# Optimization experiments

Measured on AMD Instinct MI355X. Metric: run time of the kernel, lower is better.

## Reference

```python
import jax, jax.numpy as jnp
import numpy as np

HID = 2048      # hidden_size
NH = 16         # num_attention_heads
QLR = 1536      # q_lora_rank
KVLR = 512      # kv_lora_rank
DN = 128        # qk_nope_head_dim
DR = 64         # qk_rope_head_dim
DQK = DN + DR   # qk_head_dim = 192
DV = 128        # v_head_dim
EPS = 1e-6
THETA = 10000.0
B, T = 2, 2048


def rmsnorm(x, scale):
    return x * jax.lax.rsqrt(jnp.mean(x * x, axis=-1, keepdims=True) + EPS) * scale


def rope(x, positions):
    # x: [B, T, h, d]; NeoX-style rotate-half RoPE on the rope slice only
    d = x.shape[-1]
    inv_freq = 1.0 / (THETA ** (jnp.arange(0, d, 2, dtype=jnp.float32) / d))
    ang = positions.astype(jnp.float32)[..., None] * inv_freq       # [B, T, d/2]
    cos = jnp.cos(ang)[:, :, None, :]
    sin = jnp.sin(ang)[:, :, None, :]
    x1, x2 = jnp.split(x, 2, axis=-1)
    return jnp.concatenate([x1 * cos - x2 * sin, x2 * cos + x1 * sin], axis=-1).astype(x.dtype)


def setup_inputs() -> dict:
    key = jax.random.key(0)
    ks = jax.random.split(key, 8)
    s = 0.02
    x = jax.random.normal(ks[0], (B, T, HID), dtype=jnp.float32)
    attention_mask = jnp.ones((B, T), dtype=bool)
    positions = jnp.broadcast_to(jnp.arange(T, dtype=jnp.int32), (B, T))
    wqa = jax.random.normal(ks[1], (HID, QLR), dtype=jnp.float32) * s
    qa_scale = jnp.ones((QLR,), dtype=jnp.float32)
    wqb = jax.random.normal(ks[2], (QLR, NH * DQK), dtype=jnp.float32) * s
    wkva = jax.random.normal(ks[3], (HID, KVLR + DR), dtype=jnp.float32) * s
    kva_scale = jnp.ones((KVLR,), dtype=jnp.float32)
    wkvb = jax.random.normal(ks[4], (KVLR, NH * (DN + DV)), dtype=jnp.float32) * s
    wo = jax.random.normal(ks[5], (NH * DV, HID), dtype=jnp.float32) * s
    return {"x": x, "attention_mask": attention_mask, "positions": positions,
            "wqa": wqa, "qa_scale": qa_scale, "wqb": wqb,
            "wkva": wkva, "kva_scale": kva_scale, "wkvb": wkvb, "wo": wo}


def reference(x, attention_mask, positions, wqa, qa_scale, wqb, wkva, kva_scale, wkvb, wo):
    Bv, Tv, _ = x.shape
    # low-rank Q: hid -> q_lora_rank -> rmsnorm -> heads*qk_head_dim
    q = (rmsnorm(x @ wqa, qa_scale) @ wqb).reshape(Bv, Tv, NH, DQK)
    q_pass, q_rot = q[..., :DN], q[..., DN:]
    # compressed KV + shared rope key
    ckv = x @ wkva                                    # [B, T, KVLR + DR]
    kv_lat, k_rot = ckv[..., :KVLR], ckv[..., KVLR:].reshape(Bv, Tv, 1, DR)
    kv = (rmsnorm(kv_lat, kva_scale) @ wkvb).reshape(Bv, Tv, NH, DN + DV)
    k_pass, v = kv[..., :DN], kv[..., DN:]
    # decoupled RoPE on rope slice only
    q_rot = rope(q_rot, positions)
    k_rot = jnp.broadcast_to(rope(k_rot, positions), (Bv, Tv, NH, DR))
    q = jnp.concatenate([q_pass, q_rot], axis=-1)     # [B, T, H, 192]
    k = jnp.concatenate([k_pass, k_rot], axis=-1)
    # masked causal SDPA; v padding in the original is a no-op mathematically
    scale = DQK ** -0.5
    scores = jnp.einsum('bqhd,bkhd->bhqk', q, k) * scale
    causal = jnp.tril(jnp.ones((Tv, Tv), dtype=bool))
    mask = causal[None, None, :, :] & attention_mask[:, None, None, :].astype(bool)
    scores = jnp.where(mask, scores, jnp.finfo(scores.dtype).min)
    probs = jax.nn.softmax(scores, axis=-1)
    out = jnp.einsum('bhqk,bkhd->bqhd', probs, v).reshape(Bv, Tv, NH * DV)
    return out @ wo
```

## Files before the change

### kernel.cpp

```cpp
#include <hip/hip_runtime.h>
#include <math.h>
#include <stdint.h>

#define NHEAD 16
#define HIDDIM 2048
#define QLRANK 1536
#define KVRANK 512
#define DROT 64
#define BB 2
#define TT 2048
#define BTOK (BB*TT)
#define NPROJ 2304
#define CKV0 1536
#define ROT0 2048

typedef __bf16 bf16x8 __attribute__((ext_vector_type(8)));
typedef __bf16 bf16x4 __attribute__((ext_vector_type(4)));
typedef float f32x4 __attribute__((ext_vector_type(4)));
typedef uint16_t u16;
typedef uint32_t u32;

__device__ __forceinline__ u16 f2bf(float f) {
  union { float f; uint32_t u; } v; v.f = f;
  uint32_t r = v.u + 0x7fffu + ((v.u >> 16) & 1u);
  return (u16)(r >> 16);
}
__device__ __forceinline__ float bf2f(u16 h) {
  union { uint32_t u; float f; } v; v.u = ((uint32_t)h) << 16;
  return v.f;
}

__device__ __forceinline__ void gload_lds16(const u16* g, u16* l) {
  __builtin_amdgcn_global_load_lds(
      (const __attribute__((address_space(1))) uint32_t*)g,
      (__attribute__((address_space(3))) uint32_t*)l, 16, 0, 0);
}

__global__ __launch_bounds__(256) void cvt_f32_bf16(const float* __restrict__ in,
                                                    u16* __restrict__ out, int n) {
  int idx = (blockIdx.x * 256 + threadIdx.x) * 8;
  if (idx >= n) return;
  f32x4 a = *(const f32x4*)&in[idx];
  f32x4 b = *(const f32x4*)&in[idx + 4];
  union { f32x4 q; u16 e[8]; } w;
#pragma unroll
  for (int j = 0; j < 4; ++j) { w.e[j] = f2bf(a[j]); w.e[4 + j] = f2bf(b[j]); }
  *(f32x4*)&out[idx] = w.q;
}

__global__ __launch_bounds__(256) void transpose_w(const float* __restrict__ W,
                                                   u16* __restrict__ Wt,
                                                   int K, int N, int Npad, float scale,
                                                   const float* __restrict__ svec) {
  __shared__ float tile[32][33];
  int k0 = blockIdx.x * 32, n0 = blockIdx.y * 32;
  int tx = threadIdx.x, ty = threadIdx.y;
#pragma unroll
  for (int r = 0; r < 32; r += 8) {
    int k = k0 + ty + r, n = n0 + tx;
    tile[ty + r][tx] = (k < K && n < N) ? W[(size_t)k * N + n] : 0.f;
  }
  __syncthreads();
  float sv = scale * (svec ? svec[k0 + tx] : 1.f);
#pragma unroll
  for (int r = 0; r < 32; r += 8) {
    int n = n0 + ty + r, k = k0 + tx;
    if (n < Npad && k < K) Wt[(size_t)n * K + k] = f2bf(tile[tx][ty + r] * sv);
  }
}

template<int D>
__global__ __launch_bounds__(256) void row_invrms(const u16* __restrict__ in, int stride,
                                                  float* __restrict__ out) {
  const int row = blockIdx.x;
  const int tid = threadIdx.x;
  constexpr int NC = D / 8;
  float ss = 0.f;
  if (tid < NC) {
    union { f32x4 q; u16 e[8]; } t;
    t.q = *(const f32x4*)&in[(size_t)row * stride + tid * 8];
#pragma unroll
    for (int j = 0; j < 8; ++j) { float v = bf2f(t.e[j]); ss += v * v; }
  }
#pragma unroll
  for (int off = 1; off < 64; off <<= 1) ss += __shfl_xor(ss, off);
  __shared__ float red[4];
  if ((tid & 63) == 0) red[tid >> 6] = ss;
  __syncthreads();
  if (tid == 0)
    out[row] = rsqrtf((red[0] + red[1] + red[2] + red[3]) / (float)D + 1e-6f);
}

template<int OUTF32>
__global__ __launch_bounds__(512, 2) void gemm256(const u16* __restrict__ A, int lda,
                                                  const u16* __restrict__ Bt,
                                                  void* __restrict__ Cv, int ldc,
                                                  const float* __restrict__ rowscale,
                                                  int K) {
  __shared__ __align__(16) u16 S[2][2][16384];
  const int tid = threadIdx.x, lane = tid & 63, wave = tid >> 6;
  const int l15 = lane & 15, l4 = lane >> 4;
  const int bm = blockIdx.y * 256, bn = blockIdx.x * 256;
  const int wm = wave >> 2, wn = wave & 3;

  const int rlo = lane >> 3;
  const int cbase = ((lane & 7) * 8) ^ ((lane >> 5) << 4);
  const u16* src[8];
  u16* dst[8];
#pragma unroll
  for (int j = 0; j < 8; ++j) {
    int gj = wave * 8 + j;
    if (gj < 32) {
      src[j] = A + (size_t)(bm + gj * 8 + rlo) * lda + cbase;
      dst[j] = &S[0][0][0] + gj * 512;
    } else {
      src[j] = Bt + (size_t)(bn + (gj - 32) * 8 + rlo) * K + cbase;
      dst[j] = &S[0][1][0] + (gj - 32) * 512;
    }
  }

  const int flip = ((l15 >> 2) & 1) << 5;
  const char* Sa0 = (const char*)&S[0][0][0] + wm * 16384;
  const char* Sb0 = (const char*)&S[0][1][0] + (wn >> 1) * 16384;
  const int arow0 = l15 * 128 + l4 * 16;
  const int brow0 = ((wn & 1) * 64 + l15) * 128 + l4 * 16;

  f32x4 acc[8][4] = {};
  const int nt = K >> 6;

#pragma unroll
  for (int j = 0; j < 8; ++j) gload_lds16(src[j], dst[j]);
#pragma unroll
  for (int j = 0; j < 8; ++j) gload_lds16(src[j] + 64, dst[j] + 32768);
  asm volatile("s_waitcnt vmcnt(8)" ::: "memory");
  __builtin_amdgcn_s_barrier();
  __builtin_amdgcn_sched_barrier(0);

  for (int t = 0; t < nt; ++t) {
    const char* Sab = Sa0 + (t & 1) * 65536;
    const char* Sbb = Sb0 + (t & 1) * 65536;
    bf16x8 bfr[4][2];
#pragma unroll
    for (int fn = 0; fn < 4; ++fn) {
      bfr[fn][0] = *(const bf16x8*)(Sbb + ((brow0 + fn * 2048) ^ flip));
      bfr[fn][1] = *(const bf16x8*)(Sbb + ((brow0 + fn * 2048 + 64) ^ flip));
    }
#pragma unroll
    for (int q = 0; q < 4; ++q) {
      bf16x8 a0[2], a1[2];
#pragma unroll
      for (int m2 = 0; m2 < 2; ++m2) {
        const int fm = q * 2 + m2;
        bf16x8 x0 = *(const bf16x8*)(Sab + ((arow0 + fm * 2048) ^ flip));
        bf16x8 x1 = *(const bf16x8*)(Sab + ((arow0 + fm * 2048 + 64) ^ flip));
        a0[m2] = x0; a1[m2] = x1;
      }
      __builtin_amdgcn_s_setprio(1);
#pragma unroll
      for (int m2 = 0; m2 < 2; ++m2)
#pragma unroll
        for (int fn = 0; fn < 4; ++fn) {
          f32x4 c = acc[q * 2 + m2][fn];
          c = __builtin_amdgcn_mfma_f32_16x16x32_bf16(a0[m2], bfr[fn][0], c, 0, 0, 0);
          c = __builtin_amdgcn_mfma_f32_16x16x32_bf16(a1[m2], bfr[fn][1], c, 0, 0, 0);
          acc[q * 2 + m2][fn] = c;
        }
      __builtin_amdgcn_s_setprio(0);
    }
    if (t + 1 < nt) {
      __builtin_amdgcn_s_barrier();
      __builtin_amdgcn_sched_barrier(0);
      if (t + 2 < nt) {
        const int koff = (t + 2) * 64;
#pragma unroll
        for (int j = 0; j < 8; ++j) gload_lds16(src[j] + koff, dst[j] + (t & 1) * 32768);
        asm volatile("s_waitcnt vmcnt(8)" ::: "memory");
      } else {
        asm volatile("s_waitcnt vmcnt(0)" ::: "memory");
      }
      __builtin_amdgcn_s_barrier();
      __builtin_amdgcn_sched_barrier(0);
    }
  }

  const int row0 = bm + wm * 128 + l4 * 4;
  const int col0 = bn + wn * 64 + l15;
#pragma unroll
  for (int fm = 0; fm < 8; ++fm) {
    float rs[4] = {1.f, 1.f, 1.f, 1.f};
    if (rowscale) {
#pragma unroll
      for (int i = 0; i < 4; ++i) rs[i] = rowscale[row0 + fm * 16 + i];
    }
#pragma unroll
    for (int fn = 0; fn < 4; ++fn)
#pragma unroll
      for (int i = 0; i < 4; ++i) {
        size_t idx = (size_t)(row0 + fm * 16 + i) * ldc + (col0 + fn * 16);
        float v = acc[fm][fn][i] * rs[i];
        if (OUTF32) ((float*)Cv)[idx] = v;
        else        ((u16*)Cv)[idx] = f2bf(v);
      }
  }
}

__global__ __launch_bounds__(256) void rope_table(const int* __restrict__ positions,
                                                  float2* __restrict__ tab) {
  int idx = blockIdx.x * 256 + threadIdx.x;
  if (idx >= BTOK * 32) return;
  int bt = idx >> 5, i = idx & 31;
  float invf = powf(10000.0f, -(float)i / 32.0f);
  float ang = (float)positions[bt] * invf;
  tab[idx] = make_float2(cosf(ang), sinf(ang));
}

__global__ __launch_bounds__(256) void rope_q(u16* __restrict__ q,
                                              const float2* __restrict__ tab) {
  int idx = blockIdx.x * 256 + threadIdx.x;
  if (idx >= BTOK * NHEAD * 32) return;
  int i = idx & 31;
  int h = (idx >> 5) & 15;
  int bt = idx >> 9;
  u16* p = q + (size_t)bt * 3072 + h * 192 + 128;
  float x1 = bf2f(p[i]), x2 = bf2f(p[32 + i]);
  float2 cs = tab[bt * 32 + i];
  p[i] = f2bf(x1 * cs.x - x2 * cs.y);
  p[32 + i] = f2bf(x2 * cs.x + x1 * cs.y);
}

__global__ __launch_bounds__(256) void assemble_k(const u16* __restrict__ kv,
                                                  const u16* __restrict__ proj,
                                                  const float2* __restrict__ tab,
                                                  u16* __restrict__ kf) {
  int bt = blockIdx.x;
  __shared__ __align__(16) u16 krot[64];
  int t = threadIdx.x;
  if (t < 64) {
    int i = t & 31;
    float2 cs = tab[bt * 32 + i];
    float x1 = bf2f(proj[(size_t)bt * NPROJ + ROT0 + i]);
    float x2 = bf2f(proj[(size_t)bt * NPROJ + ROT0 + 32 + i]);
    krot[t] = f2bf((t < 32) ? (x1 * cs.x - x2 * cs.y) : (x2 * cs.x + x1 * cs.y));
  }
  __syncthreads();
  for (int c = t; c < 16 * 24; c += 256) {
    int h = c / 24, seg = c % 24;
    u16* dst = kf + (size_t)bt * 3072 + h * 192 + seg * 8;
    if (seg < 16)
      *(f32x4*)dst = *(const f32x4*)&kv[(size_t)bt * 4096 + h * 256 + seg * 8];
    else
      *(f32x4*)dst = *(const f32x4*)&krot[(seg - 16) * 8];
  }
}

__device__ const int8_t JOB_QT[24] = {15,15,7,14,14,13,13,6,12,12,11,11,5,10,10,9,9,4,8,8,3,2,1,0};
__device__ const int8_t JOB_PC[24] = { 0, 1,2, 0, 1, 0, 1,2, 0, 1, 0, 1,2, 0, 1,0,1,2,0,1,2,2,2,2};

__global__ __launch_bounds__(256, 2) void attn_fwd4(const u16* __restrict__ Q,
                                                    const u16* __restrict__ Kf,
                                                    const u16* __restrict__ KV,
                                                    u16* __restrict__ O,
                                                    u16* __restrict__ Opart,
                                                    float2* __restrict__ ml) {
  __shared__ __align__(16) u16 Ks[64 * 192];
  __shared__ __align__(16) u16 Vs[64 * 128];

  const int tid = threadIdx.x, lane = tid & 63, wave = tid >> 6;
  const int l15 = lane & 15, l4 = lane >> 4;
  const int jobrank = blockIdx.x >> 5;
  const int bh = blockIdx.x & 31;
  const int qt = JOB_QT[jobrank];
  const int piece = JOB_PC[jobrank];
  const int q0 = qt * 128;
  const int b = bh >> 4, h = bh & 15;
  const int wq0 = q0 + wave * 32;

  bf16x8 qf[2][6];
#pragma unroll
  for (int m = 0; m < 2; ++m) {
    const u16* qp = Q + (size_t)(b * TT + wq0 + m * 16 + l15) * 3072 + h * 192 + l4 * 8;
#pragma unroll
    for (int kk = 0; kk < 6; ++kk) qf[m][kk] = *(const bf16x8*)(qp + kk * 32);
  }

  int ksrc[6];
#pragma unroll
  for (int j = 0; j < 6; ++j) {
    int o = (wave * 6 + j) * 1024 + lane * 16;
    int row = o / 384, col = o % 384;
    int scol = col ^ ((row & 7) << 4);
    ksrc[j] = row * 3072 + (scol >> 1);
  }
  int vsrc[4];
#pragma unroll
  for (int j = 0; j < 4; ++j) {
    int lam = (wave * 4 + j) * 512 + lane * 8;
    int kap = ((lam >> 6) & 15) * 4 + ((lam >> 4) & 3);
    int key = ((kap >> 5) & 1) * 32 + ((kap >> 2) & 3) * 8 + ((kap >> 4) & 1) * 4 + (kap & 3);
    int dv  = (lam >> 10) * 16 + (lam & 15);
    vsrc[j] = key * 4096 + dv;
  }
  const u16* Kbase = Kf + (size_t)(b * TT) * 3072 + h * 192;
  const u16* Vbase = KV + (size_t)(b * TT) * 4096 + h * 256 + 128;
  u16* KsW = Ks + (wave * 6) * 512;
  u16* VsW = Vs + (wave * 4) * 512;
  const unsigned vs_base = (unsigned)(uintptr_t)(&Vs[0]);

  f32x4 o_acc[2][8] = {};
  float m_r[2], l_r[2];
#pragma unroll
  for (int m = 0; m < 2; ++m) { m_r[m] = -INFINITY; l_r[m] = 0.f; }

  const int kt0 = (piece == 1) ? (qt + 1) : 0;
  const int kt1 = (piece == 0) ? (qt + 1) : (2 * qt + 2);

  for (int kt = kt0; kt < kt1; ++kt) {
    __syncthreads();
    const u16* Kt = Kbase + (size_t)(kt * 64) * 3072;
    const u16* Vt = Vbase + (size_t)(kt * 64) * 4096;
#pragma unroll
    for (int j = 0; j < 6; ++j) gload_lds16(Kt + ksrc[j], KsW + j * 512);
#pragma unroll
    for (int j = 0; j < 4; ++j) gload_lds16(Vt + vsrc[j], VsW + j * 512);
    __syncthreads();

    if (kt * 64 > wq0 + 31) continue;
    const int kt64 = kt * 64;

    f32x4 s[2][4] = {};
    __builtin_amdgcn_s_setprio(1);
#pragma unroll
    for (int n = 0; n < 4; ++n) {
      const int krow = n * 16 + l15;
      const int swz = (l15 & 7) << 3;
#pragma unroll
      for (int kk = 0; kk < 6; ++kk) {
        bf16x8 kb = *(const bf16x8*)&Ks[krow * 192 + ((kk * 32 + l4 * 8) ^ swz)];
        s[0][n] = __builtin_amdgcn_mfma_f32_16x16x32_bf16(kb, qf[0][kk], s[0][n], 0, 0, 0);
        s[1][n] = __builtin_amdgcn_mfma_f32_16x16x32_bf16(kb, qf[1][kk], s[1][n], 0, 0, 0);
      }
    }
    __builtin_amdgcn_s_setprio(0);

    u32 pk[2][4][2];
#pragma unroll
    for (int m = 0; m < 2; ++m) {
      const int qrow = wq0 + m * 16 + l15;
      const bool needmask = (kt64 + 63) > (wq0 + m * 16);
      if (needmask) {
#pragma unroll
        for (int n = 0; n < 4; ++n)
#pragma unroll
          for (int i = 0; i < 4; ++i)
            if (kt64 + n * 16 + l4 * 4 + i > qrow) s[m][n][i] = -INFINITY;
      }
      float pmax = -INFINITY;
#pragma unroll
      for (int n = 0; n < 4; ++n)
#pragma unroll
        for (int i = 0; i < 4; ++i) pmax = fmaxf(pmax, s[m][n][i]);
      pmax = fmaxf(pmax, __shfl_xor(pmax, 16));
      pmax = fmaxf(pmax, __shfl_xor(pmax, 32));

      if (!__all(pmax - m_r[m] <= 8.f)) {
        float mn = fmaxf(m_r[m], pmax);
        float alpha = __expf(m_r[m] - mn);
        m_r[m] = mn;
        l_r[m] *= alpha;
        float ab[4];
#pragma unroll
        for (int i = 0; i < 4; ++i) ab[i] = __shfl(alpha, l4 * 4 + i);
#pragma unroll
        for (int n = 0; n < 8; ++n)
#pragma unroll
          for (int i = 0; i < 4; ++i) o_acc[m][n][i] *= ab[i];
      }

      float psum = 0.f;
#pragma unroll
      for (int n = 0; n < 4; ++n) {
        float p0 = __expf(s[m][n][0] - m_r[m]);
        float p1 = __expf(s[m][n][1] - m_r[m]);
        float p2 = __expf(s[m][n][2] - m_r[m]);
        float p3 = __expf(s[m][n][3] - m_r[m]);
        psum += (p0 + p1) + (p2 + p3);
        union { u32 u; __bf16 e[2]; } a, c;
        a.e[0] = (__bf16)p0; a.e[1] = (__bf16)p1;
        c.e[0] = (__bf16)p2; c.e[1] = (__bf16)p3;
        pk[m][n][0] = a.u;
        pk[m][n][1] = c.u;
      }
      psum += __shfl_xor(psum, 16);
      psum += __shfl_xor(psum, 32);
      l_r[m] += psum;
    }

#pragma unroll
    for (int kk = 0; kk < 2; ++kk) {
      bf16x8 pa[2];
#pragma unroll
      for (int m = 0; m < 2; ++m) {
        union { u32 w[4]; bf16x8 v; } uu;
#pragma unroll
        for (int t = 0; t < 4; ++t) {
          int src = l15 + ((2 * (l4 & 1) + (t >> 1)) << 4);
          u32 a0 = __shfl(pk[m][2 * kk + 0][t & 1], src);
          u32 a1 = __shfl(pk[m][2 * kk + 1][t & 1], src);
          uu.w[t] = (l4 & 2) ? a1 : a0;
        }
        pa[m] = uu.v;
      }
      const unsigned va = vs_base + kk * 1024 + lane * 8;
#pragma unroll
      for (int g = 0; g < 2; ++g) {
        union { uint2 u; bf16x4 b; } lo[4], hi[4];
#pragma unroll
        for (int n = 0; n < 4; ++n) {
          unsigned a0 = va + (g * 4 + n) * 2048;
          asm volatile("ds_read_b64_tr_b16 %0, %1" : "=v"(lo[n].u) : "v"(a0));
          asm volatile("ds_read_b64_tr_b16 %0, %1 offset:512" : "=v"(hi[n].u) : "v"(a0));
        }
        asm volatile("s_waitcnt lgkmcnt(0)" ::: "memory");
        __builtin_amdgcn_sched_barrier(0);
        __builtin_amdgcn_s_setprio(1);
#pragma unroll
        for (int n = 0; n < 4; ++n) {
          bf16x8 vb = __builtin_shufflevector(lo[n].b, hi[n].b, 0, 1, 2, 3, 4, 5, 6, 7);
          o_acc[0][g * 4 + n] = __builtin_amdgcn_mfma_f32_16x16x32_bf16(pa[0], vb, o_acc[0][g * 4 + n], 0, 0, 0);
          o_acc[1][g * 4 + n] = __builtin_amdgcn_mfma_f32_16x16x32_bf16(pa[1], vb, o_acc[1][g * 4 + n], 0, 0, 0);
        }
        __builtin_amdgcn_s_setprio(0);
      }
    }
  }

  if (piece == 2) {
#pragma unroll
    for (int m = 0; m < 2; ++m) {
      float inv = 1.f / l_r[m];
      float li[4];
#pragma unroll
      for (int i = 0; i < 4; ++i) li[i] = __shfl(inv, l4 * 4 + i);
#pragma unroll
      for (int n = 0; n < 8; ++n)
#pragma unroll
        for (int i = 0; i < 4; ++i) {
          int r = wq0 + m * 16 + l4 * 4 + i;
          O[(size_t)(b * TT + r) * 2048 + h * 128 + n * 16 + l15] = f2bf(o_acc[m][n][i] * li[i]);
        }
    }
  } else {
    const size_t pidx = ((size_t)(qt - 8) * 32 + bh) * 2 + piece;
    u16* op = Opart + pidx * (128 * 128);
    float2* mlp = ml + pidx * 128;
#pragma unroll
    for (int m = 0; m < 2; ++m)
#pragma unroll
      for (int n = 0; n < 8; ++n)
#pragma unroll
        for (int i = 0; i < 4; ++i)
          op[(wave * 32 + m * 16 + l4 * 4 + i) * 128 + n * 16 + l15] = f2bf(o_acc[m][n][i]);
    if (l4 == 0) {
#pragma unroll
      for (int m = 0; m < 2; ++m)
        mlp[wave * 32 + m * 16 + l15] = make_float2(m_r[m], l_r[m]);
    }
  }
}

__global__ __launch_bounds__(256) void attn_combine(const u16* __restrict__ Opart,
                                                    const float2* __restrict__ ml,
                                                    u16* __restrict__ O) {
  int gid = blockIdx.x * 256 + threadIdx.x;
  int dvseg = gid & 15;
  int row = (gid >> 4) & 127;
  int bh = (gid >> 11) & 31;
  int qt8 = gid >> 16;
  size_t i1 = ((size_t)qt8 * 32 + bh) * 2;
  float2 ml1 = ml[i1 * 128 + row], ml2 = ml[(i1 + 1) * 128 + row];
  float m = fmaxf(ml1.x, ml2.x);
  float w1 = __expf(ml1.x - m), w2 = __expf(ml2.x - m);
  float inv = 1.f / (w1 * ml1.y + w2 * ml2.y);
  union { f32x4 q; u16 e[8]; } a, bq, w;
  a.q  = *(const f32x4*)&Opart[i1 * 16384 + row * 128 + dvseg * 8];
  bq.q = *(const f32x4*)&Opart[(i1 + 1) * 16384 + row * 128 + dvseg * 8];
#pragma unroll
  for (int j = 0; j < 8; ++j)
    w.e[j] = f2bf((w1 * bf2f(a.e[j]) + w2 * bf2f(bq.e[j])) * inv);
  int b = bh >> 4, h = bh & 15;
  int r = 1024 + qt8 * 128 + row;
  *(f32x4*)&O[(size_t)(b * TT + r) * 2048 + h * 128 + dvseg * 8] = w.q;
}

extern "C" void kernel_launch(void* const* d_in, const int* in_sizes, int n_in,
                              void* d_out, int out_size, void* d_ws, size_t ws_size,
                              hipStream_t stream) {
  (void)in_sizes; (void)n_in; (void)out_size; (void)ws_size;
  const float* x         = (const float*)d_in[0];
  const int*   positions = (const int*)d_in[2];
  const float* wqa       = (const float*)d_in[3];
  const float* qa_scale  = (const float*)d_in[4];
  const float* wqb       = (const float*)d_in[5];
  const float* wkva      = (const float*)d_in[6];
  const float* kva_scale = (const float*)d_in[7];
  const float* wkvb      = (const float*)d_in[8];
  const float* wo        = (const float*)d_in[9];
  float* out = (float*)d_out;

  char* wsp = (char*)d_ws;
  auto alloc = [&](size_t bytes) {
    char* p = wsp; wsp += (bytes + 255) & ~(size_t)255; return p;
  };
  u16* xb      = (u16*)alloc((size_t)BTOK * HIDDIM * 2);
  u16* proj_t  = (u16*)alloc((size_t)NPROJ * HIDDIM * 2);
  u16* wqb_t   = (u16*)alloc((size_t)3072 * QLRANK * 2);
  u16* wkvb_t  = (u16*)alloc((size_t)4096 * KVRANK * 2);
  u16* wo_t    = (u16*)alloc((size_t)HIDDIM * HIDDIM * 2);
  u16* proj    = (u16*)alloc((size_t)BTOK * NPROJ * 2);
  u16* q       = (u16*)alloc((size_t)BTOK * 3072 * 2);
  u16* kv      = (u16*)alloc((size_t)BTOK * 4096 * 2);
  u16* kf      = (u16*)alloc((size_t)BTOK * 3072 * 2);
  float2* tab  = (float2*)alloc((size_t)BTOK * 32 * 8);
  float* invq  = (float*)alloc((size_t)BTOK * 4);
  float* invkv = (float*)alloc((size_t)BTOK * 4);
  float2* mlbuf= (float2*)alloc((size_t)8 * 32 * 2 * 128 * 8);
  u16* ao = xb;
  u16* Opart = proj;

  dim3 blk(256);
  dim3 blk512(512);
  const float qscale = 0.07216878364870322f;

  cvt_f32_bf16<<<(BTOK * HIDDIM / 8 + 255) / 256, blk, 0, stream>>>(x, xb, BTOK * HIDDIM);
  {
    dim3 tb(32, 8);
    transpose_w<<<dim3(HIDDIM / 32, QLRANK / 32), tb, 0, stream>>>(wqa, proj_t, HIDDIM, QLRANK, QLRANK, 1.f, nullptr);
    transpose_w<<<dim3(HIDDIM / 32, (NPROJ - CKV0) / 32), tb, 0, stream>>>(wkva, proj_t + (size_t)CKV0 * HIDDIM, HIDDIM, 576, NPROJ - CKV0, 1.f, nullptr);
    transpose_w<<<dim3(QLRANK / 32, 3072 / 32), tb, 0, stream>>>(wqb, wqb_t, QLRANK, 3072, 3072, qscale, qa_scale);
    transpose_w<<<dim3(KVRANK / 32, 4096 / 32), tb, 0, stream>>>(wkvb, wkvb_t, KVRANK, 4096, 4096, 1.f, kva_scale);
    transpose_w<<<dim3(HIDDIM / 32, HIDDIM / 32), tb, 0, stream>>>(wo, wo_t, HIDDIM, HIDDIM, HIDDIM, 1.f, nullptr);
  }
  rope_table<<<(BTOK * 32 + 255) / 256, blk, 0, stream>>>(positions, tab);

  gemm256<0><<<dim3(NPROJ / 256, BTOK / 256), blk512, 0, stream>>>(xb, HIDDIM, proj_t, proj, NPROJ, nullptr, HIDDIM);

  row_invrms<QLRANK><<<BTOK, blk, 0, stream>>>(proj, NPROJ, invq);
  row_invrms<KVRANK><<<BTOK, blk, 0, stream>>>(proj + CKV0, NPROJ, invkv);

  gemm256<0><<<dim3(3072 / 256, BTOK / 256), blk512, 0, stream>>>(proj, NPROJ, wqb_t, q, 3072, invq, QLRANK);
  gemm256<0><<<dim3(4096 / 256, BTOK / 256), blk512, 0, stream>>>(proj + CKV0, NPROJ, wkvb_t, kv, 4096, invkv, KVRANK);

  rope_q<<<(BTOK * NHEAD * 32 + 255) / 256, blk, 0, stream>>>(q, tab);
  assemble_k<<<BTOK, blk, 0, stream>>>(kv, proj, tab, kf);

  attn_fwd4<<<dim3(24 * 32), blk, 0, stream>>>(q, kf, kv, ao, Opart, mlbuf);
  attn_combine<<<(8 * 32 * 128 * 16) / 256, blk, 0, stream>>>(Opart, mlbuf, ao);

  gemm256<1><<<dim3(HIDDIM / 256, BTOK / 256), blk512, 0, stream>>>(ao, HIDDIM, wo_t, out, HIDDIM, nullptr, HIDDIM);
}
```

Before: 374.6 us.

## Double-buffer attention K/V tiles and use 128x128 GEMM for first and output projections

Attention now keeps two LDS buffers for K and V. The next tile's loads are issued before the current tile is computed, using vmcnt waits and raw barriers instead of two __syncthreads per tile, so global-load latency overlaps with MFMA work. A new 128x128-tile, 256-thread double-buffered GEMM replaces the 256x256 gemm256 for the x projection and the output projection, giving more blocks on the small-N GEMMs. The new GEMM's LDS layout has no swizzle, so bank conflicts and a weaker pipeline than the tuned gemm256 could offset the occupancy gain. Doubling the attention LDS may also limit blocks per CU.

```diff
diff --git a/kernel.cpp b/kernel.cpp
--- a/kernel.cpp
+++ b/kernel.cpp
@@ -92,6 +92,87 @@
 }
 
 template<int OUTF32>
+__global__ __launch_bounds__(256) void gemm_bt(const u16* __restrict__ A, int lda,
+                                               const u16* __restrict__ Bt,
+                                               void* __restrict__ Cv, int ldc,
+                                               const float* __restrict__ rowscale,
+                                               int N, int K) {
+  __shared__ __align__(16) u16 As[2][128 * 32];
+  __shared__ __align__(16) u16 Bs[2][128 * 32];
+  const int tid = threadIdx.x;
+  const int lane = tid & 63;
+  const int wave = tid >> 6;
+  const int bm = blockIdx.y * 128;
+  const int bn = blockIdx.x * 128;
+  const int wr = wave >> 1;
+  const int wc = wave & 1;
+
+  f32x4 acc[4][4] = {};
+
+  const int srow = wave * 16 + (lane >> 2);
+  const int scol = (lane & 3) * 8;
+  const u16* Ag = A + (size_t)(bm + srow) * lda + scol;
+  const u16* Bg = Bt + (size_t)(bn + srow) * K + scol;
+  const int soff = (wave * 16) * 32;
+
+  const int a_off = (wr * 64 + (lane & 15)) * 32 + (lane >> 4) * 8;
+  const int b_off = (wc * 64 + (lane & 15)) * 32 + (lane >> 4) * 8;
+
+  const int nt = K >> 5;
+
+  gload_lds16(Ag, &As[0][soff]);
+  gload_lds16(Ag + (size_t)64 * lda, &As[0][soff + 64 * 32]);
+  gload_lds16(Bg, &Bs[0][soff]);
+  gload_lds16(Bg + (size_t)64 * K, &Bs[0][soff + 64 * 32]);
+  __syncthreads();
+
+  int cur = 0;
+  for (int t = 0; t < nt; ++t) {
+    if (t + 1 < nt) {
+      const int k0 = (t + 1) << 5;
+      gload_lds16(Ag + k0, &As[cur ^ 1][soff]);
+      gload_lds16(Ag + (size_t)64 * lda + k0, &As[cur ^ 1][soff + 64 * 32]);
+      gload_lds16(Bg + k0, &Bs[cur ^ 1][soff]);
+      gload_lds16(Bg + (size_t)64 * K + k0, &Bs[cur ^ 1][soff + 64 * 32]);
+    }
+    bf16x8 af[4], bfr[4];
+#pragma unroll
+    for (int m = 0; m < 4; ++m) af[m] = *(const bf16x8*)&As[cur][a_off + m * 16 * 32];
+#pragma unroll
+    for (int n = 0; n < 4; ++n) bfr[n] = *(const bf16x8*)&Bs[cur][b_off + n * 16 * 32];
+#pragma unroll
+    for (int m = 0; m < 4; ++m)
+#pragma unroll
+      for (int n = 0; n < 4; ++n)
+        acc[m][n] = __builtin_amdgcn_mfma_f32_16x16x32_bf16(af[m], bfr[n], acc[m][n], 0, 0, 0);
+    if (t + 1 < nt) {
+      __syncthreads();
+      cur ^= 1;
+    }
+  }
+
+  const int row0 = bm + wr * 64 + (lane >> 4) * 4;
+  const int col0 = bn + wc * 64 + (lane & 15);
+#pragma unroll
+  for (int m = 0; m < 4; ++m) {
+    float rs[4] = {1.f, 1.f, 1.f, 1.f};
+    if (rowscale) {
+#pragma unroll
+      for (int i = 0; i < 4; ++i) rs[i] = rowscale[row0 + m * 16 + i];
+    }
+#pragma unroll
+    for (int n = 0; n < 4; ++n)
+#pragma unroll
+      for (int i = 0; i < 4; ++i) {
+        size_t idx = (size_t)(row0 + m * 16 + i) * ldc + (col0 + n * 16);
+        float v = acc[m][n][i] * rs[i];
+        if (OUTF32) ((float*)Cv)[idx] = v;
+        else        ((u16*)Cv)[idx] = f2bf(v);
+      }
+  }
+}
+
+template<int OUTF32>
 __global__ __launch_bounds__(512, 2) void gemm256(const u16* __restrict__ A, int lda,
                                                   const u16* __restrict__ Bt,
                                                   void* __restrict__ Cv, int ldc,
@@ -151,9 +232,8 @@
 #pragma unroll
       for (int m2 = 0; m2 < 2; ++m2) {
         const int fm = q * 2 + m2;
-        bf16x8 x0 = *(const bf16x8*)(Sab + ((arow0 + fm * 2048) ^ flip));
-        bf16x8 x1 = *(const bf16x8*)(Sab + ((arow0 + fm * 2048 + 64) ^ flip));
-        a0[m2] = x0; a1[m2] = x1;
+        a0[m2] = *(const bf16x8*)(Sab + ((arow0 + fm * 2048) ^ flip));
+        a1[m2] = *(const bf16x8*)(Sab + ((arow0 + fm * 2048 + 64) ^ flip));
       }
       __builtin_amdgcn_s_setprio(1);
 #pragma unroll
@@ -256,14 +336,14 @@
 __device__ const int8_t JOB_QT[24] = {15,15,7,14,14,13,13,6,12,12,11,11,5,10,10,9,9,4,8,8,3,2,1,0};
 __device__ const int8_t JOB_PC[24] = { 0, 1,2, 0, 1, 0, 1,2, 0, 1, 0, 1,2, 0, 1,0,1,2,0,1,2,2,2,2};
 
-__global__ __launch_bounds__(256, 2) void attn_fwd4(const u16* __restrict__ Q,
+__global__ __launch_bounds__(256, 2) void attn_fwd5(const u16* __restrict__ Q,
                                                     const u16* __restrict__ Kf,
                                                     const u16* __restrict__ KV,
                                                     u16* __restrict__ O,
                                                     u16* __restrict__ Opart,
                                                     float2* __restrict__ ml) {
-  __shared__ __align__(16) u16 Ks[64 * 192];
-  __shared__ __align__(16) u16 Vs[64 * 128];
+  __shared__ __align__(16) u16 Ks[2][64 * 192];
+  __shared__ __align__(16) u16 Vs[2][64 * 128];
 
   const int tid = threadIdx.x, lane = tid & 63, wave = tid >> 6;
   const int l15 = lane & 15, l4 = lane >> 4;
@@ -302,9 +382,9 @@
   }
   const u16* Kbase = Kf + (size_t)(b * TT) * 3072 + h * 192;
   const u16* Vbase = KV + (size_t)(b * TT) * 4096 + h * 256 + 128;
-  u16* KsW = Ks + (wave * 6) * 512;
-  u16* VsW = Vs + (wave * 4) * 512;
-  const unsigned vs_base = (unsigned)(uintptr_t)(&Vs[0]);
+  const int kofsW = wave * 3072;
+  const int vofsW = wave * 2048;
+  const unsigned vs_base = (unsigned)(uintptr_t)(&Vs[0][0]);
 
   f32x4 o_acc[2][8] = {};
   float m_r[2], l_r[2];
@@ -314,15 +394,31 @@
   const int kt0 = (piece == 1) ? (qt + 1) : 0;
   const int kt1 = (piece == 0) ? (qt + 1) : (2 * qt + 2);
 
+  {
+    const u16* Kt = Kbase + (size_t)(kt0 * 64) * 3072;
+    const u16* Vt = Vbase + (size_t)(kt0 * 64) * 4096;
+#pragma unroll
+    for (int j = 0; j < 6; ++j) gload_lds16(Kt + ksrc[j], &Ks[0][kofsW + j * 512]);
+#pragma unroll
+    for (int j = 0; j < 4; ++j) gload_lds16(Vt + vsrc[j], &Vs[0][vofsW + j * 512]);
+  }
+
   for (int kt = kt0; kt < kt1; ++kt) {
-    __syncthreads();
-    const u16* Kt = Kbase + (size_t)(kt * 64) * 3072;
-    const u16* Vt = Vbase + (size_t)(kt * 64) * 4096;
-#pragma unroll
-    for (int j = 0; j < 6; ++j) gload_lds16(Kt + ksrc[j], KsW + j * 512);
-#pragma unroll
-    for (int j = 0; j < 4; ++j) gload_lds16(Vt + vsrc[j], VsW + j * 512);
-    __syncthreads();
+    const int cur = (kt - kt0) & 1;
+    __builtin_amdgcn_s_barrier();
+    if (kt + 1 < kt1) {
+      const u16* Kt = Kbase + (size_t)((kt + 1) * 64) * 3072;
+      const u16* Vt = Vbase + (size_t)((kt + 1) * 64) * 4096;
+#pragma unroll
+      for (int j = 0; j < 6; ++j) gload_lds16(Kt + ksrc[j], &Ks[cur ^ 1][kofsW + j * 512]);
+#pragma unroll
+      for (int j = 0; j < 4; ++j) gload_lds16(Vt + vsrc[j], &Vs[cur ^ 1][vofsW + j * 512]);
+      asm volatile("s_waitcnt vmcnt(10)" ::: "memory");
+    } else {
+      asm volatile("s_waitcnt vmcnt(0)" ::: "memory");
+    }
+    __builtin_amdgcn_s_barrier();
+    __builtin_amdgcn_sched_barrier(0);
 
     if (kt * 64 > wq0 + 31) continue;
     const int kt64 = kt * 64;
@@ -335,7 +431,7 @@
       const int swz = (l15 & 7) << 3;
 #pragma unroll
       for (int kk = 0; kk < 6; ++kk) {
-        bf16x8 kb = *(const bf16x8*)&Ks[krow * 192 + ((kk * 32 + l4 * 8) ^ swz)];
+        bf16x8 kb = *(const bf16x8*)&Ks[cur][krow * 192 + ((kk * 32 + l4 * 8) ^ swz)];
         s[0][n] = __builtin_amdgcn_mfma_f32_16x16x32_bf16(kb, qf[0][kk], s[0][n], 0, 0, 0);
         s[1][n] = __builtin_amdgcn_mfma_f32_16x16x32_bf16(kb, qf[1][kk], s[1][n], 0, 0, 0);
       }
@@ -410,7 +506,7 @@
         }
         pa[m] = uu.v;
       }
-      const unsigned va = vs_base + kk * 1024 + lane * 8;
+      const unsigned va = vs_base + cur * 16384 + kk * 1024 + lane * 8;
 #pragma unroll
       for (int g = 0; g < 2; ++g) {
         union { uint2 u; bf16x4 b; } lo[4], hi[4];
@@ -542,7 +638,7 @@
   }
   rope_table<<<(BTOK * 32 + 255) / 256, blk, 0, stream>>>(positions, tab);
 
-  gemm256<0><<<dim3(NPROJ / 256, BTOK / 256), blk512, 0, stream>>>(xb, HIDDIM, proj_t, proj, NPROJ, nullptr, HIDDIM);
+  gemm_bt<0><<<dim3(NPROJ / 128, BTOK / 128), blk, 0, stream>>>(xb, HIDDIM, proj_t, proj, NPROJ, nullptr, NPROJ, HIDDIM);
 
   row_invrms<QLRANK><<<BTOK, blk, 0, stream>>>(proj, NPROJ, invq);
   row_invrms<KVRANK><<<BTOK, blk, 0, stream>>>(proj + CKV0, NPROJ, invkv);
@@ -553,8 +649,8 @@
   rope_q<<<(BTOK * NHEAD * 32 + 255) / 256, blk, 0, stream>>>(q, tab);
   assemble_k<<<BTOK, blk, 0, stream>>>(kv, proj, tab, kf);
 
-  attn_fwd4<<<dim3(24 * 32), blk, 0, stream>>>(q, kf, kv, ao, Opart, mlbuf);
+  attn_fwd5<<<dim3(24 * 32), blk, 0, stream>>>(q, kf, kv, ao, Opart, mlbuf);
   attn_combine<<<(8 * 32 * 128 * 16) / 256, blk, 0, stream>>>(Opart, mlbuf, ao);
 
-  gemm256<1><<<dim3(HIDDIM / 256, BTOK / 256), blk512, 0, stream>>>(ao, HIDDIM, wo_t, out, HIDDIM, nullptr, HIDDIM);
-}
+  gemm_bt<1><<<dim3(HIDDIM / 128, BTOK / 128), blk, 0, stream>>>(ao, HIDDIM, wo_t, out, HIDDIM, nullptr, HIDDIM, HIDDIM);
+}
```

After: 350.4 us. 1.07x faster.
